# Kernel tuning notes

Hardware: AMD Instinct MI355X
Metric: run time of the kernel (lower is better)

The kernel has to match this reference:

```python
import jax, jax.numpy as jnp
import numpy as np

HIDDEN = 1024
NUM_HEAD = 16
HEAD_DIM = HIDDEN // NUM_HEAD


def setup_inputs() -> dict:
    key = jax.random.key(0)
    ks = jax.random.split(key, 9)
    B, S = 1, 4096
    scale = 1.0 / np.sqrt(HIDDEN)
    inp = {
        "x": jax.random.normal(ks[0], (B, S, HIDDEN), dtype=jnp.float32),
        "wq": jax.random.normal(ks[1], (HIDDEN, HIDDEN), dtype=jnp.float32) * scale,
        "bq": jnp.zeros((HIDDEN,), dtype=jnp.float32),
        "wk": jax.random.normal(ks[2], (HIDDEN, HIDDEN), dtype=jnp.float32) * scale,
        "bk": jnp.zeros((HIDDEN,), dtype=jnp.float32),
        "wv": jax.random.normal(ks[3], (HIDDEN, HIDDEN), dtype=jnp.float32) * scale,
        "bv": jnp.zeros((HIDDEN,), dtype=jnp.float32),
        "wo": jax.random.normal(ks[4], (HIDDEN, HIDDEN), dtype=jnp.float32) * scale,
        "bo": jnp.zeros((HIDDEN,), dtype=jnp.float32),
    }
    return inp


def reference(x, wq, bq, wk, bk, wv, bv, wo, bo):
    B, S, _ = x.shape
    # QKV projections (torch Linear: x @ W.T + b)
    def split_heads(t):
        return t.reshape(B, S, NUM_HEAD, HEAD_DIM).transpose(0, 2, 1, 3)  # [B,H,S,D]
    q = split_heads(x @ wq.T + bq)
    k = split_heads(x @ wk.T + bk)
    v = split_heads(x @ wv.T + bv)
    # scaled dot-product scores: [B,H,S,S]
    scores = jnp.einsum('bhsd,bhtd->bhst', q, k) / jnp.sqrt(jnp.float32(HEAD_DIM))
    # faithful double softmax over the key axis (no mask; dropout = eval identity)
    attn = jax.nn.softmax(scores, axis=-1)
    attn = jax.nn.softmax(attn, axis=-1)
    out = jnp.einsum('bhst,bhtd->bhsd', attn, v)  # [B,H,S,D]
    out = out.transpose(0, 2, 1, 3).reshape(B, S, HIDDEN)
    return out @ wo.T + bo
```

## Files before the change

kernel.cpp:

```cpp
#include <hip/hip_runtime.h>
#include <hip/hip_bf16.h>
#include <stdint.h>

#define S 4096
#define HID 1024
#define NH 16
#define DH 64

typedef __attribute__((ext_vector_type(8))) short short8;
typedef __attribute__((ext_vector_type(4))) float f32x4;
typedef __attribute__((ext_vector_type(16))) float f32x16;
typedef __attribute__((ext_vector_type(4))) unsigned int u32x4;

__device__ __forceinline__ unsigned short f2bf(float f) {
  unsigned int u = __builtin_bit_cast(unsigned int, f);
  u += 0x7FFF + ((u >> 16) & 1);
  return (unsigned short)(u >> 16);
}
__device__ __forceinline__ unsigned int pktrunc(float lo, float hi) {
  return __builtin_amdgcn_perm(__builtin_bit_cast(unsigned int, hi),
                               __builtin_bit_cast(unsigned int, lo), 0x07060302u);
}
__device__ __forceinline__ void gload16(const unsigned short* g, unsigned short* l) {
  __builtin_amdgcn_global_load_lds((const __attribute__((address_space(1))) unsigned int*)g,
                                   (__attribute__((address_space(3))) unsigned int*)l, 16, 0, 0);
}

__global__ __launch_bounds__(256) void cast_kernel(
    const float* __restrict__ x,  const float* __restrict__ wq,
    const float* __restrict__ wk, const float* __restrict__ wv,
    const float* __restrict__ wo,
    unsigned short* __restrict__ xb,  unsigned short* __restrict__ wqb,
    unsigned short* __restrict__ wkb, unsigned short* __restrict__ wvb,
    unsigned short* __restrict__ wob)
{
  int y = blockIdx.y;
  const float* src; unsigned short* dst; int n;
  if      (y == 0) { src = x;  dst = xb;  n = S * HID; }
  else if (y == 1) { src = wq; dst = wqb; n = HID * HID; }
  else if (y == 2) { src = wk; dst = wkb; n = HID * HID; }
  else if (y == 3) { src = wv; dst = wvb; n = HID * HID; }
  else             { src = wo; dst = wob; n = HID * HID; }
  int i = (blockIdx.x * 256 + threadIdx.x) * 4;
  if (i < n) {
    float4 v = *reinterpret_cast<const float4*>(src + i);
    ushort4 o;
    o.x = f2bf(v.x); o.y = f2bf(v.y); o.z = f2bf(v.z); o.w = f2bf(v.w);
    *reinterpret_cast<ushort4*>(dst + i) = o;
  }
}

__device__ __forceinline__ void gemm128(
    const unsigned short* __restrict__ A, const unsigned short* __restrict__ W,
    unsigned short* As, unsigned short* Bs, f32x4 acc[4][4], int row0, int col0)
{
  const int tid = threadIdx.x;
  const int wave = tid >> 6, lane = tid & 63, quad = lane >> 4, l16 = lane & 15;
  const int wr = (wave >> 1) * 64, wc = (wave & 1) * 64;
  const int srow = lane >> 2, sseg = lane & 3;
  const f32x4 z = {0.f, 0.f, 0.f, 0.f};
  #pragma unroll
  for (int i = 0; i < 4; i++)
    #pragma unroll
    for (int j = 0; j < 4; j++) acc[i][j] = z;

  for (int k0 = 0; k0 < HID; k0 += 32) {
    __syncthreads();
    #pragma unroll
    for (int c = 0; c < 2; c++) {
      const int rbase = c * 64 + wave * 16;
      gload16(A + (size_t)(row0 + rbase + srow) * HID + k0 + sseg * 8, As + rbase * 32);
      gload16(W + (size_t)(col0 + rbase + srow) * HID + k0 + sseg * 8, Bs + rbase * 32);
    }
    __syncthreads();

    short8 af[4], bfr[4];
    #pragma unroll
    for (int i = 0; i < 4; i++)
      af[i] = *reinterpret_cast<const short8*>(As + (wr + i * 16 + l16) * 32 + quad * 8);
    #pragma unroll
    for (int j = 0; j < 4; j++)
      bfr[j] = *reinterpret_cast<const short8*>(Bs + (wc + j * 16 + l16) * 32 + quad * 8);
    #pragma unroll
    for (int i = 0; i < 4; i++)
      #pragma unroll
      for (int j = 0; j < 4; j++)
        acc[i][j] = __builtin_amdgcn_mfma_f32_16x16x32_bf16(af[i], bfr[j], acc[i][j], 0, 0, 0);
  }
}

__global__ __launch_bounds__(256) void qkv_gemm_kernel(
    const unsigned short* __restrict__ X,
    const unsigned short* __restrict__ Wq, const unsigned short* __restrict__ Wk,
    const unsigned short* __restrict__ Wv,
    const float* __restrict__ bq, const float* __restrict__ bk, const float* __restrict__ bv,
    unsigned short* __restrict__ Qo, unsigned short* __restrict__ K2o, unsigned short* __restrict__ Vbo)
{
  __shared__ unsigned short As[128 * 32];
  __shared__ unsigned short Bs[128 * 32];
  const int zsel = blockIdx.z;
  const unsigned short* W = (zsel == 0) ? Wq : (zsel == 1) ? Wk : Wv;
  const float* bias        = (zsel == 0) ? bq : (zsel == 1) ? bk : bv;
  const int row0 = blockIdx.x * 128, col0 = blockIdx.y * 128;
  f32x4 acc[4][4];
  gemm128(X, W, As, Bs, acc, row0, col0);

  const int tid = threadIdx.x;
  const int wave = tid >> 6, lane = tid & 63, quad = lane >> 4, l16 = lane & 15;
  const int wr = (wave >> 1) * 64, wc = (wave & 1) * 64;

  if (zsel == 0) {
    const float osc = 0.18033688011112042f;
    #pragma unroll
    for (int j = 0; j < 4; j++) {
      int n = col0 + wc + j * 16 + l16;
      float bb = bias[n];
      int h = n >> 6, d = n & 63;
      #pragma unroll
      for (int i = 0; i < 4; i++)
        #pragma unroll
        for (int rr = 0; rr < 4; rr++) {
          int s = row0 + wr + i * 16 + quad * 4 + rr;
          Qo[(size_t)(h * S + s) * DH + d] = f2bf((acc[i][j][rr] + bb) * osc);
        }
    }
  } else if (zsel == 1) {
    #pragma unroll
    for (int j = 0; j < 4; j++) {
      int n = col0 + wc + j * 16 + l16;
      float bb = bias[n];
      int h = n >> 6, dh = n & 63;
      int c = dh >> 4, hfk = (dh >> 3) & 1, j8 = dh & 7;
      #pragma unroll
      for (int i = 0; i < 4; i++)
        #pragma unroll
        for (int rr = 0; rr < 4; rr++) {
          int s = row0 + wr + i * 16 + quad * 4 + rr;
          int g = s >> 5, l32k = s & 31;
          K2o[((size_t)((h * 128 + g) * 4 + c) * 64 + hfk * 32 + l32k) * 8 + j8] =
              f2bf(acc[i][j][rr] + bb);
        }
    }
  } else {
    #pragma unroll
    for (int j = 0; j < 4; j++) {
      int n = col0 + wc + j * 16 + l16;
      float bb = bias[n];
      int h = n >> 6, dh = n & 63;
      int ng = dh >> 5, l32v = dh & 31;
      int hf_v = quad & 1, jj0 = (quad >> 1) * 4;
      #pragma unroll
      for (int i = 0; i < 4; i++) {
        int gt = (row0 + wr + i * 16) >> 5;
        int grp = i & 1;
        ushort4 pv;
        pv.x = f2bf(acc[i][j][0] + bb); pv.y = f2bf(acc[i][j][1] + bb);
        pv.z = f2bf(acc[i][j][2] + bb); pv.w = f2bf(acc[i][j][3] + bb);
        *reinterpret_cast<ushort4*>(
            Vbo + ((size_t)(((h * 128 + gt) * 2 + grp) * 2 + ng) * 64 + hf_v * 32 + l32v) * 8 + jj0) = pv;
      }
    }
  }
}

__global__ __launch_bounds__(256) void out_gemm_kernel(
    const unsigned short* __restrict__ A, const unsigned short* __restrict__ W,
    const float* __restrict__ be, float* __restrict__ dst)
{
  __shared__ unsigned short As[128 * 32];
  __shared__ unsigned short Bs[128 * 32];
  const int row0 = blockIdx.x * 128, col0 = blockIdx.y * 128;
  f32x4 acc[4][4];
  gemm128(A, W, As, Bs, acc, row0, col0);

  const int tid = threadIdx.x;
  const int wave = tid >> 6, lane = tid & 63, quad = lane >> 4, l16 = lane & 15;
  const int wr = (wave >> 1) * 64, wc = (wave & 1) * 64;
  #pragma unroll
  for (int j = 0; j < 4; j++) {
    int n = col0 + wc + j * 16 + l16;
    float bb = be[n];
    #pragma unroll
    for (int i = 0; i < 4; i++)
      #pragma unroll
      for (int rr = 0; rr < 4; rr++) {
        int s = row0 + wr + i * 16 + quad * 4 + rr;
        dst[(size_t)s * HID + n] = acc[i][j][rr] + bb;
      }
  }
}

__global__ __launch_bounds__(256) void vsum_kernel(
    const unsigned short* __restrict__ Vb, float* __restrict__ VsumP)
{
  __shared__ float red[256];
  const int p = blockIdx.x, h = blockIdx.y, tid = threadIdx.x;
  const int d = tid & 63, chunk = tid >> 6;
  const int ng = d >> 5, l32 = d & 31;
  float s = 0.f;
  for (int m = 0; m < 4; m++) {
    int gt = p * 16 + chunk * 4 + m;
    #pragma unroll
    for (int grp = 0; grp < 2; grp++)
      #pragma unroll
      for (int hf = 0; hf < 2; hf++) {
        uint4 u = *reinterpret_cast<const uint4*>(
            Vb + ((size_t)(((h * 128 + gt) * 2 + grp) * 2 + ng) * 64 + hf * 32 + l32) * 8);
        const unsigned int w[4] = {u.x, u.y, u.z, u.w};
        #pragma unroll
        for (int q = 0; q < 4; q++) {
          s += __builtin_bit_cast(float, w[q] << 16);
          s += __builtin_bit_cast(float, w[q] & 0xFFFF0000u);
        }
      }
  }
  red[tid] = s;
  __syncthreads();
  if (tid < 64)
    VsumP[p * 1024 + h * 64 + tid] = red[tid] + red[64 + tid] + red[128 + tid] + red[192 + tid];
}

__global__ __launch_bounds__(256) void biasfold_kernel(
    const float* __restrict__ VsumP, const float* __restrict__ wo,
    const float* __restrict__ bo, float* __restrict__ be)
{
  const int n = blockIdx.x * 4 + (threadIdx.x >> 6);
  const int l = threadIdx.x & 63;
  float acc = 0.f;
  #pragma unroll
  for (int i = 0; i < 16; i++) {
    float vs = 0.f;
    #pragma unroll
    for (int p = 0; p < 8; p++) vs += VsumP[p * 1024 + l + 64 * i];
    acc += vs * wo[(size_t)n * HID + l + 64 * i];
  }
  #pragma unroll
  for (int off = 32; off >= 1; off >>= 1) acc += __shfl_xor(acc, off);
  if (l == 0) be[n] = bo[n] + acc * (1.f / 4097.f);
}

__global__ __launch_bounds__(256, 4) void attn_kernel(
    const unsigned short* __restrict__ Q, const unsigned short* __restrict__ K2,
    const unsigned short* __restrict__ Vb, unsigned short* __restrict__ OUT)
{
  __shared__ float Ol[2][32][64];
  __shared__ float Z1l[128];

  const int lin = blockIdx.y * 64 + blockIdx.x;
  const int xcd = lin & 7, idx = lin >> 3;
  const int h = xcd * 2 + (idx >> 6);
  const int q0 = (idx & 63) * 64;

  const int tid = threadIdx.x;
  const int wave = tid >> 6, lane = tid & 63, hf = lane >> 5, l32 = lane & 31;
  const int qc = wave & 1, ks = wave >> 1;

  short8 qf[4];
  {
    const unsigned short* qrow = Q + (size_t)(h * S + q0 + qc * 32 + l32) * DH;
    #pragma unroll
    for (int c = 0; c < 4; c++)
      qf[c] = *reinterpret_cast<const short8*>(qrow + c * 16 + hf * 8);
  }

  float z1p = 0.f;
  f32x16 Oa[2];
  #pragma unroll
  for (int ng = 0; ng < 2; ng++)
    #pragma unroll
    for (int r = 0; r < 16; r++) Oa[ng][r] = 0.f;

  const unsigned short* Kb = K2 + (size_t)h * 128 * 4 * 64 * 8;
  const unsigned short* Vbb = Vb + (size_t)h * 128 * 4 * 64 * 8;

  const int g0 = ks * 64, g1 = g0 + 64;
  for (int g = g0; g < g1; g++) {
    short8 kf[4];
    #pragma unroll
    for (int c = 0; c < 4; c++)
      kf[c] = *reinterpret_cast<const short8*>(Kb + ((size_t)(g * 4 + c) * 64 + lane) * 8);
    short8 vfr[2][2];
    #pragma unroll
    for (int grp = 0; grp < 2; grp++)
      #pragma unroll
      for (int ng = 0; ng < 2; ng++)
        vfr[grp][ng] = *reinterpret_cast<const short8*>(
            Vbb + ((size_t)((g * 2 + grp) * 2 + ng) * 64 + lane) * 8);

    f32x16 acc;
    #pragma unroll
    for (int r = 0; r < 16; r++) acc[r] = 0.f;
    #pragma unroll
    for (int c = 0; c < 4; c++)
      acc = __builtin_amdgcn_mfma_f32_32x32x16_bf16(kf[c], qf[c], acc, 0, 0, 0);

    unsigned int D[8];
    #pragma unroll
    for (int m = 0; m < 8; m++) {
      float t0 = __builtin_amdgcn_exp2f(acc[2 * m]);
      float t1 = __builtin_amdgcn_exp2f(acc[2 * m + 1]);
      z1p += t0 + t1;
      D[m] = pktrunc(t0, t1);
    }
    u32x4 d0 = {D[0], D[1], D[2], D[3]};
    u32x4 d1 = {D[4], D[5], D[6], D[7]};
    short8 A0 = __builtin_bit_cast(short8, d0);
    short8 A1 = __builtin_bit_cast(short8, d1);

    Oa[0] = __builtin_amdgcn_mfma_f32_32x32x16_bf16(A0, vfr[0][0], Oa[0], 0, 0, 0);
    Oa[1] = __builtin_amdgcn_mfma_f32_32x32x16_bf16(A0, vfr[0][1], Oa[1], 0, 0, 0);
    Oa[0] = __builtin_amdgcn_mfma_f32_32x32x16_bf16(A1, vfr[1][0], Oa[0], 0, 0, 0);
    Oa[1] = __builtin_amdgcn_mfma_f32_32x32x16_bf16(A1, vfr[1][1], Oa[1], 0, 0, 0);
  }

  {
    float z1 = z1p + __shfl_xor(z1p, 32);
    if (hf == 0) Z1l[ks * 64 + qc * 32 + l32] = z1;
  }
  if (ks == 0) {
    #pragma unroll
    for (int reg = 0; reg < 16; reg++) {
      const int row = (reg & 3) + 8 * (reg >> 2) + 4 * hf;
      #pragma unroll
      for (int ng = 0; ng < 2; ng++)
        Ol[qc][row][ng * 32 + l32] = Oa[ng][reg];
    }
  }
  __syncthreads();
  if (ks == 1) {
    #pragma unroll
    for (int reg = 0; reg < 16; reg++) {
      const int row = (reg & 3) + 8 * (reg >> 2) + 4 * hf;
      const int ql = qc * 32 + row;
      const float rz = 1.f / ((Z1l[ql] + Z1l[64 + ql]) * 4097.f);
      const int s = q0 + ql;
      #pragma unroll
      for (int ng = 0; ng < 2; ng++) {
        const float o = Ol[qc][row][ng * 32 + l32] + Oa[ng][reg];
        OUT[(size_t)s * HID + h * DH + ng * 32 + l32] = f2bf(o * rz);
      }
    }
  }
}

extern "C" void kernel_launch(void* const* d_in, const int* in_sizes, int n_in,
                              void* d_out, int out_size, void* d_ws, size_t ws_size,
                              hipStream_t stream) {
  const float* x  = (const float*)d_in[0];
  const float* wq = (const float*)d_in[1];
  const float* bq = (const float*)d_in[2];
  const float* wk = (const float*)d_in[3];
  const float* bk = (const float*)d_in[4];
  const float* wv = (const float*)d_in[5];
  const float* bv = (const float*)d_in[6];
  const float* wo = (const float*)d_in[7];
  const float* bo = (const float*)d_in[8];
  float* out = (float*)d_out;

  char* ws = (char*)d_ws;
  unsigned short* xb  = (unsigned short*)(ws);
  unsigned short* wqb = (unsigned short*)(ws + (8u  << 20));
  unsigned short* wkb = (unsigned short*)(ws + (10u << 20));
  unsigned short* wvb = (unsigned short*)(ws + (12u << 20));
  unsigned short* wob = (unsigned short*)(ws + (14u << 20));
  unsigned short* qw  = (unsigned short*)(ws + (16u << 20));
  unsigned short* k2  = (unsigned short*)(ws + (24u << 20));
  unsigned short* vb  = (unsigned short*)(ws + (32u << 20));
  float* vsump        = (float*)(ws + (40u << 20));
  float* be           = (float*)(ws + (40u << 20) + 65536);
  unsigned short* aw  = xb;

  cast_kernel<<<dim3(4096, 5), 256, 0, stream>>>(x, wq, wk, wv, wo, xb, wqb, wkb, wvb, wob);
  qkv_gemm_kernel<<<dim3(32, 8, 3), 256, 0, stream>>>(xb, wqb, wkb, wvb, bq, bk, bv, qw, k2, vb);
  vsum_kernel<<<dim3(8, 16), 256, 0, stream>>>(vb, vsump);
  biasfold_kernel<<<dim3(256), 256, 0, stream>>>(vsump, wo, bo, be);
  attn_kernel<<<dim3(64, 16), 256, 0, stream>>>(qw, k2, vb, aw);
  out_gemm_kernel<<<dim3(32, 8, 1), 256, 0, stream>>>(aw, wob, be, out);
}
```

Baseline: 248.1 us.

## Stage K/V tiles in LDS with double-buffered async global-to-LDS loads

```diff
diff --git a/kernel.cpp b/kernel.cpp
--- a/kernel.cpp
+++ b/kernel.cpp
@@ -243,8 +243,10 @@
     const unsigned short* __restrict__ Q, const unsigned short* __restrict__ K2,
     const unsigned short* __restrict__ Vb, unsigned short* __restrict__ OUT)
 {
-  __shared__ float Ol[2][32][64];
-  __shared__ float Z1l[128];
+  __shared__ unsigned short Tiles[2][2][2][2048];
+  float* Ol  = reinterpret_cast<float*>(&Tiles[0][0][0][0]);
+  float* Z1l = reinterpret_cast<float*>(
+      reinterpret_cast<char*>(&Tiles[0][0][0][0]) + 16384);
 
   const int lin = blockIdx.y * 64 + blockIdx.x;
   const int xcd = lin & 7, idx = lin >> 3;
@@ -273,19 +275,40 @@
   const unsigned short* Kb = K2 + (size_t)h * 128 * 4 * 64 * 8;
   const unsigned short* Vbb = Vb + (size_t)h * 128 * 4 * 64 * 8;
 
-  const int g0 = ks * 64, g1 = g0 + 64;
-  for (int g = g0; g < g1; g++) {
+  const int sks = wave >> 1, sv = wave & 1;
+  const unsigned short* gsrc =
+      (sv ? Vbb : Kb) + (size_t)sks * 64 * 2048 + (size_t)lane * 8;
+  unsigned short* ldsbase = &Tiles[0][sks][sv][0];
+
+  #pragma unroll
+  for (int i = 0; i < 4; i++)
+    gload16(gsrc + i * 512, ldsbase + i * 512);
+  __syncthreads();
+
+  int buf = 0;
+  for (int gl = 0; gl < 64; gl++) {
+    if (gl + 1 < 64) {
+      const unsigned short* s = gsrc + (size_t)(gl + 1) * 2048;
+      unsigned short* d = ldsbase + (buf ^ 1) * (2 * 2 * 2048);
+      #pragma unroll
+      for (int i = 0; i < 4; i++)
+        gload16(s + i * 512, d + i * 512);
+    }
+
+    const unsigned short* TK = &Tiles[buf][ks][0][0];
+    const unsigned short* TV = &Tiles[buf][ks][1][0];
+
     short8 kf[4];
     #pragma unroll
     for (int c = 0; c < 4; c++)
-      kf[c] = *reinterpret_cast<const short8*>(Kb + ((size_t)(g * 4 + c) * 64 + lane) * 8);
+      kf[c] = *reinterpret_cast<const short8*>(TK + (c * 64 + lane) * 8);
     short8 vfr[2][2];
     #pragma unroll
     for (int grp = 0; grp < 2; grp++)
       #pragma unroll
       for (int ng = 0; ng < 2; ng++)
         vfr[grp][ng] = *reinterpret_cast<const short8*>(
-            Vbb + ((size_t)((g * 2 + grp) * 2 + ng) * 64 + lane) * 8);
+            TV + ((grp * 2 + ng) * 64 + lane) * 8);
 
     f32x16 acc;
     #pragma unroll
@@ -311,6 +334,9 @@
     Oa[1] = __builtin_amdgcn_mfma_f32_32x32x16_bf16(A0, vfr[0][1], Oa[1], 0, 0, 0);
     Oa[0] = __builtin_amdgcn_mfma_f32_32x32x16_bf16(A1, vfr[1][0], Oa[0], 0, 0, 0);
     Oa[1] = __builtin_amdgcn_mfma_f32_32x32x16_bf16(A1, vfr[1][1], Oa[1], 0, 0, 0);
+
+    __syncthreads();
+    buf ^= 1;
   }
 
   {
@@ -323,7 +349,7 @@
       const int row = (reg & 3) + 8 * (reg >> 2) + 4 * hf;
       #pragma unroll
       for (int ng = 0; ng < 2; ng++)
-        Ol[qc][row][ng * 32 + l32] = Oa[ng][reg];
+        Ol[(qc * 32 + row) * 64 + ng * 32 + l32] = Oa[ng][reg];
     }
   }
   __syncthreads();
@@ -336,7 +362,7 @@
       const int s = q0 + ql;
       #pragma unroll
       for (int ng = 0; ng < 2; ng++) {
-        const float o = Ol[qc][row][ng * 32 + l32] + Oa[ng][reg];
+        const float o = Ol[(qc * 32 + row) * 64 + ng * 32 + l32] + Oa[ng][reg];
         OUT[(size_t)s * HID + h * DH + ng * 32 + l32] = f2bf(o * rz);
       }
     }
```

After: 252.7 us. No clear change (+1.9%).

## Double-buffer K/V tiles in LDS via async global_load_lds in attention loop

Applied to the files above, without the earlier changes.

```diff
diff --git a/kernel.cpp b/kernel.cpp
--- a/kernel.cpp
+++ b/kernel.cpp
@@ -8,6 +8,7 @@
 #define DH 64
 
 typedef __attribute__((ext_vector_type(8))) short short8;
+typedef __attribute__((ext_vector_type(2))) float f32x2;
 typedef __attribute__((ext_vector_type(4))) float f32x4;
 typedef __attribute__((ext_vector_type(16))) float f32x16;
 typedef __attribute__((ext_vector_type(4))) unsigned int u32x4;
@@ -239,12 +240,64 @@
   if (l == 0) be[n] = bo[n] + acc * (1.f / 4097.f);
 }
 
+struct AttnState {
+  short8 qf[4];
+  f32x16 Oa[2];
+  f32x16 zacc;
+  f32x2  zp;
+};
+
+template<int BUF>
+__device__ __forceinline__ void attn_compute(
+    const unsigned short* kbase, const unsigned short* vbase, AttnState& st)
+{
+  short8 kf[4], vfr[4];
+  #pragma unroll
+  for (int c = 0; c < 4; c++)
+    kf[c] = *reinterpret_cast<const short8*>(kbase + BUF * 8192 + c * 512);
+  #pragma unroll
+  for (int w = 0; w < 4; w++)
+    vfr[w] = *reinterpret_cast<const short8*>(vbase + BUF * 8192 + w * 512);
+
+  f32x16 acc = __builtin_amdgcn_mfma_f32_32x32x16_bf16(kf[0], st.qf[0], st.zacc, 0, 0, 0);
+  #pragma unroll
+  for (int c = 1; c < 4; c++)
+    acc = __builtin_amdgcn_mfma_f32_32x32x16_bf16(kf[c], st.qf[c], acc, 0, 0, 0);
+
+  unsigned int D[8];
+  #pragma unroll
+  for (int m = 0; m < 8; m++) {
+    float t0 = __builtin_amdgcn_exp2f(acc[2 * m]);
+    float t1 = __builtin_amdgcn_exp2f(acc[2 * m + 1]);
+    f32x2 t = {t0, t1};
+    st.zp += t;
+    D[m] = pktrunc(t0, t1);
+  }
+  u32x4 d0 = {D[0], D[1], D[2], D[3]};
+  u32x4 d1 = {D[4], D[5], D[6], D[7]};
+  short8 A0 = __builtin_bit_cast(short8, d0);
+  short8 A1 = __builtin_bit_cast(short8, d1);
+
+  st.Oa[0] = __builtin_amdgcn_mfma_f32_32x32x16_bf16(A0, vfr[0], st.Oa[0], 0, 0, 0);
+  st.Oa[1] = __builtin_amdgcn_mfma_f32_32x32x16_bf16(A0, vfr[1], st.Oa[1], 0, 0, 0);
+  st.Oa[0] = __builtin_amdgcn_mfma_f32_32x32x16_bf16(A1, vfr[2], st.Oa[0], 0, 0, 0);
+  st.Oa[1] = __builtin_amdgcn_mfma_f32_32x32x16_bf16(A1, vfr[3], st.Oa[1], 0, 0, 0);
+}
+
+__device__ __forceinline__ void stage4(const unsigned short* gs, unsigned short* ldst) {
+  #pragma unroll
+  for (int i = 0; i < 4; i++)
+    gload16(gs + i * 512, ldst + i * 512);
+}
+
 __global__ __launch_bounds__(256, 4) void attn_kernel(
     const unsigned short* __restrict__ Q, const unsigned short* __restrict__ K2,
     const unsigned short* __restrict__ Vb, unsigned short* __restrict__ OUT)
 {
-  __shared__ float Ol[2][32][64];
-  __shared__ float Z1l[128];
+  __shared__ unsigned short T[2][2][2][2048];
+  float* Ol  = reinterpret_cast<float*>(&T[0][0][0][0]);
+  float* Z1l = reinterpret_cast<float*>(
+      reinterpret_cast<char*>(&T[0][0][0][0]) + 16384);
 
   const int lin = blockIdx.y * 64 + blockIdx.x;
   const int xcd = lin & 7, idx = lin >> 3;
@@ -255,65 +308,49 @@
   const int wave = tid >> 6, lane = tid & 63, hf = lane >> 5, l32 = lane & 31;
   const int qc = wave & 1, ks = wave >> 1;
 
-  short8 qf[4];
+  AttnState st;
   {
     const unsigned short* qrow = Q + (size_t)(h * S + q0 + qc * 32 + l32) * DH;
     #pragma unroll
     for (int c = 0; c < 4; c++)
-      qf[c] = *reinterpret_cast<const short8*>(qrow + c * 16 + hf * 8);
-  }
-
-  float z1p = 0.f;
-  f32x16 Oa[2];
-  #pragma unroll
-  for (int ng = 0; ng < 2; ng++)
-    #pragma unroll
-    for (int r = 0; r < 16; r++) Oa[ng][r] = 0.f;
+      st.qf[c] = *reinterpret_cast<const short8*>(qrow + c * 16 + hf * 8);
+  }
+  #pragma unroll
+  for (int r = 0; r < 16; r++) { st.zacc[r] = 0.f; st.Oa[0][r] = 0.f; st.Oa[1][r] = 0.f; }
+  st.zp = (f32x2){0.f, 0.f};
 
   const unsigned short* Kb = K2 + (size_t)h * 128 * 4 * 64 * 8;
   const unsigned short* Vbb = Vb + (size_t)h * 128 * 4 * 64 * 8;
 
-  const int g0 = ks * 64, g1 = g0 + 64;
-  for (int g = g0; g < g1; g++) {
-    short8 kf[4];
-    #pragma unroll
-    for (int c = 0; c < 4; c++)
-      kf[c] = *reinterpret_cast<const short8*>(Kb + ((size_t)(g * 4 + c) * 64 + lane) * 8);
-    short8 vfr[2][2];
-    #pragma unroll
-    for (int grp = 0; grp < 2; grp++)
-      #pragma unroll
-      for (int ng = 0; ng < 2; ng++)
-        vfr[grp][ng] = *reinterpret_cast<const short8*>(
-            Vbb + ((size_t)((g * 2 + grp) * 2 + ng) * 64 + lane) * 8);
-
-    f32x16 acc;
-    #pragma unroll
-    for (int r = 0; r < 16; r++) acc[r] = 0.f;
-    #pragma unroll
-    for (int c = 0; c < 4; c++)
-      acc = __builtin_amdgcn_mfma_f32_32x32x16_bf16(kf[c], qf[c], acc, 0, 0, 0);
-
-    unsigned int D[8];
-    #pragma unroll
-    for (int m = 0; m < 8; m++) {
-      float t0 = __builtin_amdgcn_exp2f(acc[2 * m]);
-      float t1 = __builtin_amdgcn_exp2f(acc[2 * m + 1]);
-      z1p += t0 + t1;
-      D[m] = pktrunc(t0, t1);
-    }
-    u32x4 d0 = {D[0], D[1], D[2], D[3]};
-    u32x4 d1 = {D[4], D[5], D[6], D[7]};
-    short8 A0 = __builtin_bit_cast(short8, d0);
-    short8 A1 = __builtin_bit_cast(short8, d1);
-
-    Oa[0] = __builtin_amdgcn_mfma_f32_32x32x16_bf16(A0, vfr[0][0], Oa[0], 0, 0, 0);
-    Oa[1] = __builtin_amdgcn_mfma_f32_32x32x16_bf16(A0, vfr[0][1], Oa[1], 0, 0, 0);
-    Oa[0] = __builtin_amdgcn_mfma_f32_32x32x16_bf16(A1, vfr[1][0], Oa[0], 0, 0, 0);
-    Oa[1] = __builtin_amdgcn_mfma_f32_32x32x16_bf16(A1, vfr[1][1], Oa[1], 0, 0, 0);
-  }
+  const int sks = wave >> 1, sv = wave & 1;
+  const unsigned short* gs =
+      (sv ? Vbb : Kb) + (size_t)sks * 64 * 2048 + (size_t)lane * 8;
+  unsigned short* stT0 = &T[0][sks][sv][0];
+  unsigned short* stT1 = &T[1][sks][sv][0];
+
+  const unsigned short* kbase = &T[0][ks][0][0] + lane * 8;
+  const unsigned short* vbase = &T[0][ks][1][0] + lane * 8;
+
+  stage4(gs, stT0);
+  gs += 2048;
+  __syncthreads();
+
+  for (int t = 0; t < 31; t++) {
+    stage4(gs, stT1); gs += 2048;
+    attn_compute<0>(kbase, vbase, st);
+    __syncthreads();
+    stage4(gs, stT0); gs += 2048;
+    attn_compute<1>(kbase, vbase, st);
+    __syncthreads();
+  }
+  stage4(gs, stT1);
+  attn_compute<0>(kbase, vbase, st);
+  __syncthreads();
+  attn_compute<1>(kbase, vbase, st);
+  __syncthreads();
 
   {
+    float z1p = st.zp[0] + st.zp[1];
     float z1 = z1p + __shfl_xor(z1p, 32);
     if (hf == 0) Z1l[ks * 64 + qc * 32 + l32] = z1;
   }
@@ -323,7 +360,7 @@
       const int row = (reg & 3) + 8 * (reg >> 2) + 4 * hf;
       #pragma unroll
       for (int ng = 0; ng < 2; ng++)
-        Ol[qc][row][ng * 32 + l32] = Oa[ng][reg];
+        Ol[(qc * 32 + row) * 64 + ng * 32 + l32] = st.Oa[ng][reg];
     }
   }
   __syncthreads();
@@ -336,7 +373,7 @@
       const int s = q0 + ql;
       #pragma unroll
       for (int ng = 0; ng < 2; ng++) {
-        const float o = Ol[qc][row][ng * 32 + l32] + Oa[ng][reg];
+        const float o = Ol[(qc * 32 + row) * 64 + ng * 32 + l32] + st.Oa[ng][reg];
         OUT[(size_t)s * HID + h * DH + ng * 32 + l32] = f2bf(o * rz);
       }
     }
```

Result: faster. 242.5 us (-2.2%).
